# Performance work log

Hardware: AMD Instinct MI355X
Metric: run time of the kernel (lower is better)

The kernel has to match this reference:

```python
import jax, jax.numpy as jnp
import numpy as np

K = 20
EPS = 1e-5


def graph_feature(x, k=K):
    # x: [B, C, N] -> [B, 2C, N, k] (DGCNN edge features)
    xt = jnp.transpose(x, (0, 2, 1))                      # [B, N, C]
    sq = jnp.sum(xt * xt, axis=-1)                        # [B, N]
    inner = jnp.einsum('bnc,bmc->bnm', xt, xt)            # [B, N, N]
    neg_dist = 2.0 * inner - sq[:, :, None] - sq[:, None, :]
    idx = jax.lax.top_k(neg_dist, k)[1]                   # [B, N, k]
    nbr = jax.vmap(lambda f, i: f[i])(xt, idx)            # [B, N, k, C]
    ctr = jnp.broadcast_to(xt[:, :, None, :], nbr.shape)
    feat = jnp.concatenate([nbr - ctr, ctr], axis=-1)     # [B, N, k, 2C]
    return jnp.transpose(feat, (0, 3, 1, 2))              # [B, 2C, N, k]


def conv_bn_relu(x, W, g, b):
    # 1x1 conv (channel matmul) + BatchNorm (batch stats, training mode) + ReLU
    y = jnp.einsum('oc,bcnk->bonk', W, x)
    m = jnp.mean(y, axis=(0, 2, 3), keepdims=True)
    v = jnp.var(y, axis=(0, 2, 3), keepdims=True)
    yn = (y - m) * jax.lax.rsqrt(v + EPS)
    return jax.nn.relu(yn * g[None, :, None, None] + b[None, :, None, None])


def setup_inputs() -> dict:
    key = jax.random.key(0)
    ks = jax.random.split(key, 12)
    d = {'x': jax.random.normal(ks[0], (8, 3, 2048), dtype=jnp.float32)}
    chans = [(6, 64), (64, 64), (64, 128), (128, 256), (512, 512)]
    for i, (cin, cout) in enumerate(chans):
        d[f'W{i+1}'] = jax.random.normal(ks[i + 1], (cout, cin), dtype=jnp.float32) * (1.0 / np.sqrt(cin))
        d[f'g{i+1}'] = jnp.ones((cout,), dtype=jnp.float32)
        d[f'b{i+1}'] = jnp.zeros((cout,), dtype=jnp.float32)
    return d


def reference(x, W1, g1, b1, W2, g2, b2, W3, g3, b3, W4, g4, b4, W5, g5, b5):
    B, C, N = x.shape
    h = graph_feature(x)                                  # [B, 6, N, k]
    h = conv_bn_relu(h, W1, g1, b1)
    x1 = jnp.max(h, axis=-1, keepdims=True)               # [B, 64, N, 1]
    h = conv_bn_relu(h, W2, g2, b2)
    x2 = jnp.max(h, axis=-1, keepdims=True)
    h = conv_bn_relu(h, W3, g3, b3)
    x3 = jnp.max(h, axis=-1, keepdims=True)
    h = conv_bn_relu(h, W4, g4, b4)
    x4 = jnp.max(h, axis=-1, keepdims=True)
    cat = jnp.concatenate([x1, x2, x3, x4], axis=1)       # [B, 512, N, 1]
    out = conv_bn_relu(cat, W5, g5, b5)                   # [B, 512, N, 1]
    return out.reshape(B, -1, N)
```

## Files before the change

### kernel.cpp

```cpp
#include <hip/hip_runtime.h>
#include <hip/hip_bf16.h>

typedef _Float16 f16;
typedef _Float16 f16x8 __attribute__((ext_vector_type(8)));
typedef _Float16 f16x4 __attribute__((ext_vector_type(4)));
typedef float    f32x4 __attribute__((ext_vector_type(4)));
typedef unsigned long long u64;

constexpr int NB  = 8;
constexpr int NPT = 2048;
constexpr int KK  = 20;
constexpr int PT  = NB * NPT * KK;
constexpr int BNP = NB * NPT;
constexpr float EPS_BN = 1e-5f;
constexpr int NREP = 64;

constexpr size_t OFF_IDX = 0;
constexpr size_t OFF_WT1 = OFF_IDX + (size_t)BNP * KK * 4;
constexpr size_t OFF_WH2 = OFF_WT1 + 384 * 4;
constexpr size_t OFF_WH3 = OFF_WH2 + 4096 * 2;
constexpr size_t OFF_WH4 = OFF_WH3 + 8192 * 2;
constexpr size_t OFF_WH5 = OFF_WH4 + 32768 * 2;
constexpr size_t OFF_ST  = OFF_WH5 + 262144 * 2;
constexpr size_t OFF_SS  = OFF_ST + 5 * 1024 * 4;
constexpr size_t OFF_CAT = OFF_SS + 5 * 1024 * 4;
constexpr size_t OFF_Y3  = OFF_CAT + (size_t)BNP * 512 * 2;
constexpr size_t OFF_Y1  = OFF_Y3 + (size_t)PT * 64 * 2;
constexpr size_t OFF_Y2  = OFF_Y3 + (size_t)PT * 128 * 2;
constexpr size_t OFF_REP = OFF_Y2 + (size_t)PT * 64 * 2;
constexpr size_t WS_NEED = OFF_REP + (size_t)NREP * 1024 * 4;

__global__ void marker_kernel(float* __restrict__ out, float v) {
    if (threadIdx.x == 0 && blockIdx.x == 0) out[0] = v;
}

__device__ __forceinline__ void gload16(const f16* g, f16* ldsbase) {
    __builtin_amdgcn_global_load_lds(
        (const __attribute__((address_space(1))) void*)g,
        (__attribute__((address_space(3))) void*)ldsbase, 16, 0, 0);
}

__global__ __launch_bounds__(256) void prep_weights(
        const float* __restrict__ W1, const float* __restrict__ W2,
        const float* __restrict__ W3, const float* __restrict__ W4,
        const float* __restrict__ W5,
        float* __restrict__ wt1, f16* __restrict__ wh2, f16* __restrict__ wh3,
        f16* __restrict__ wh4, f16* __restrict__ wh5) {
    int i = blockIdx.x * 256 + threadIdx.x;
    if (i < 384)    { int o = i / 6, c = i - o * 6; wt1[c * 64 + o] = W1[i]; }
    if (i < 4096)   wh2[i] = (f16)W2[i];
    if (i < 8192)   wh3[i] = (f16)W3[i];
    if (i < 32768)  wh4[i] = (f16)W4[i];
    if (i < 262144) wh5[i] = (f16)W5[i];
}

__device__ __forceinline__ float distf(const float* __restrict__ xb, int m,
                                       float xn0, float xn1, float xn2, float sqn) {
    float xm0 = xb[m], xm1 = xb[NPT + m], xm2 = xb[2 * NPT + m];
    float dot = xn0 * xm0 + xn1 * xm1 + xn2 * xm2;
    float sqm = xm0 * xm0 + xm1 * xm1 + xm2 * xm2;
    return 2.f * dot - sqn - sqm;
}
__device__ __forceinline__ u64 mkkey(float d, int m) {
    unsigned u = __float_as_uint(d);
    u = (u & 0x80000000u) ? ~u : (u | 0x80000000u);
    return ((u64)u << 32) | (unsigned)(2047 - m);
}
__device__ __forceinline__ int key2m(u64 k) { return 2047 - (int)(k & 0xFFFFFFFFull); }

__device__ __forceinline__ void qins(u64 k, u64& q0, u64& q1, u64& q2, u64& q3, u64& spill) {
    bool c0 = k > q0, c1 = k > q1, c2 = k > q2, c3 = k > q3;
    u64 drop = c3 ? q3 : k;
    spill = spill > drop ? spill : drop;
    q3 = c2 ? q2 : (c3 ? k : q3);
    q2 = c1 ? q1 : (c2 ? k : q2);
    q1 = c0 ? q0 : (c1 ? k : q1);
    q0 = c0 ? k  : q0;
}

__global__ __launch_bounds__(256) void knn_kernel(const float* __restrict__ x,
                                                  int* __restrict__ idxo) {
    const int lane = threadIdx.x & 63;
    const int wid  = threadIdx.x >> 6;
    const int r    = blockIdx.x * 4 + wid;
    const int b    = r >> 11;
    const int n    = r & 2047;
    const float* xb = x + b * (3 * NPT);

    const float xn0 = xb[n], xn1 = xb[NPT + n], xn2 = xb[2 * NPT + n];
    const float sqn = xn0 * xn0 + xn1 * xn1 + xn2 * xn2;

    u64 q0 = 0, q1 = 0, q2 = 0, q3 = 0, spill = 0;
#pragma unroll
    for (int i = 0; i < 32; ++i) {
        int m = i * 64 + lane;
        qins(mkkey(distf(xb, m, xn0, xn1, xn2, sqn), m), q0, q1, q2, q3, spill);
    }

    __shared__ int cand[4][32];
    int C;

    unsigned lo = 0u, hi = 0xFFFFFFFFu;
#pragma unroll 1
    for (int it = 0; it < 32 && lo < hi; ++it) {
        unsigned span = hi - lo;
        unsigned mid  = lo + (span >> 1) + (span & 1);
        u64 M = (u64)mid << 32;
        int cnt = __popcll(__ballot(q0 >= M)) + __popcll(__ballot(q1 >= M))
                + __popcll(__ballot(q2 >= M)) + __popcll(__ballot(q3 >= M));
        if (cnt >= 26) lo = mid; else hi = mid - 1;
    }
    const u64 T64 = (u64)lo << 32;

    u64 b0 = __ballot(q0 >= T64), b1 = __ballot(q1 >= T64);
    u64 b2 = __ballot(q2 >= T64), b3 = __ballot(q3 >= T64);
    int n0 = __popcll(b0), n1 = __popcll(b1), n2 = __popcll(b2), n3 = __popcll(b3);
    C = n0 + n1 + n2 + n3;
    bool conflict = (__ballot(spill >= T64) != 0ull) || (C > 32);

    if (!conflict) {
        u64 ltm = (1ull << lane) - 1ull;
        if (q0 >= T64) cand[wid][__popcll(b0 & ltm)] = key2m(q0);
        if (q1 >= T64) cand[wid][n0 + __popcll(b1 & ltm)] = key2m(q1);
        if (q2 >= T64) cand[wid][n0 + n1 + __popcll(b2 & ltm)] = key2m(q2);
        if (q3 >= T64) cand[wid][n0 + n1 + n2 + __popcll(b3 & ltm)] = key2m(q3);
    } else {
        C = 26;
#pragma unroll 1
        for (int t = 0; t < 26; ++t) {
            u64 v = q0;
#pragma unroll
            for (int s = 1; s < 64; s <<= 1) {
                u64 ov = __shfl_xor(v, s);
                if (ov > v) v = ov;
            }
            if (lane == 0) cand[wid][t] = key2m(v);
            if (q0 == v) {
                q0 = q1; q1 = q2; q2 = q3; q3 = 0;
                if (!(q0 > spill)) {
                    q0 = q1 = q2 = q3 = 0; spill = 0;
                    for (int ii = 0; ii < 32; ++ii) {
                        int mr = ii * 64 + lane;
                        u64 kr = mkkey(distf(xb, mr, xn0, xn1, xn2, sqn), mr);
                        if (kr < v) qins(kr, q0, q1, q2, q3, spill);
                    }
                }
            }
        }
    }
    __syncthreads();

    int mm = (lane < C) ? cand[wid][lane] : 0;
    const double dxn0 = (double)xn0, dxn1 = (double)xn1, dxn2 = (double)xn2;
    const double dsqn = dxn0 * dxn0 + dxn1 * dxn1 + dxn2 * dxn2;
    double xm0 = (double)xb[mm], xm1 = (double)xb[NPT + mm], xm2 = (double)xb[2 * NPT + mm];
    double ddot = dxn0 * xm0 + dxn1 * xm1 + dxn2 * xm2;
    double dsqm = xm0 * xm0 + xm1 * xm1 + xm2 * xm2;
    double dd   = 2.0 * ddot - dsqn - dsqm;

    int rank = 0;
#pragma unroll 1
    for (int s = 0; s < C; ++s) {
        double ds = __shfl(dd, s);
        int    ms = __shfl(mm, s);
        if (ds > dd || (ds == dd && ms < mm)) ++rank;
    }
    if (lane < C && rank < KK) idxo[rank * BNP + r] = mm;
}

__global__ __launch_bounds__(256) void conv1_kernel(const float* __restrict__ x,
                                                    const int* __restrict__ idx,
                                                    const float* __restrict__ Wt,
                                                    f16* __restrict__ y,
                                                    float* __restrict__ strep) {
    const int tid = threadIdx.x, lane = tid & 63, wid = tid >> 6;
    int p = blockIdx.x * 256 + tid;
    int r = p & (BNP - 1);
    int n = r & 2047;
    int b = r >> 11;
    int m = idx[p];
    const float* xb = x + b * (3 * NPT);
    float f3 = xb[n], f4 = xb[NPT + n], f5 = xb[2 * NPT + n];
    float f0 = xb[m] - f3, f1 = xb[NPT + m] - f4, f2 = xb[2 * NPT + m] - f5;
    float fv[6] = { f0, f1, f2, f3, f4, f5 };

    float acc[64];
#pragma unroll
    for (int o = 0; o < 64; ++o) acc[o] = 0.f;
#pragma unroll
    for (int c = 0; c < 6; ++c) {
        float hv = fv[c];
#pragma unroll
        for (int o = 0; o < 64; ++o) acc[o] = fmaf(Wt[c * 64 + o], hv, acc[o]);
    }
    f16* yp = y + (size_t)p * 64;
#pragma unroll
    for (int o = 0; o < 64; ++o) yp[o] = (f16)acc[o];

    __shared__ float lsum[4][64], lsq[4][64];
#pragma unroll
    for (int o = 0; o < 64; ++o) {
        float s = acc[o], q = acc[o] * acc[o];
#pragma unroll
        for (int off = 32; off >= 1; off >>= 1) { s += __shfl_xor(s, off); q += __shfl_xor(q, off); }
        if (lane == 0) { lsum[wid][o] = s; lsq[wid][o] = q; }
    }
    __syncthreads();
    float* rep = strep + ((blockIdx.x & (NREP - 1)) << 10);
    if (tid < 64) {
        atomicAdd(rep + tid,       lsum[0][tid] + lsum[1][tid] + lsum[2][tid] + lsum[3][tid]);
        atomicAdd(rep + 512 + tid, lsq[0][tid] + lsq[1][tid] + lsq[2][tid] + lsq[3][tid]);
    }
}

template<int CIN, int OBW>
__global__ __launch_bounds__(256) void conv_mfma_kernel(const f16* __restrict__ h,
                                                        const f16* __restrict__ W,
                                                        const float* __restrict__ scshIn,
                                                        f16* __restrict__ y,
                                                        float* __restrict__ strep) {
    constexpr int COUT = OBW * 64;
    const int tid = threadIdx.x, lane = tid & 63, wid = tid >> 6;
    const int lr = lane & 15, lg = lane >> 4;
    const int p0 = blockIdx.x * (256 / OBW) + (wid / OBW) * 64;
    const int ob = (wid & (OBW - 1)) * 64;

    f16x8 Bn[CIN / 32][4];
#pragma unroll
    for (int kt = 0; kt < CIN / 32; ++kt) {
        const int koff = kt * 32 + lg * 8;
        const float4 s0 = *(const float4*)(scshIn + koff);
        const float4 s1 = *(const float4*)(scshIn + koff + 4);
        const float4 h0 = *(const float4*)(scshIn + 512 + koff);
        const float4 h1 = *(const float4*)(scshIn + 512 + koff + 4);
        const float scr[8] = { s0.x, s0.y, s0.z, s0.w, s1.x, s1.y, s1.z, s1.w };
        const float shr[8] = { h0.x, h0.y, h0.z, h0.w, h1.x, h1.y, h1.z, h1.w };
#pragma unroll
        for (int pt = 0; pt < 4; ++pt) {
            f16x8 raw = *(const f16x8*)(h + (size_t)(p0 + pt * 16 + lr) * CIN + koff);
            f16x8 Bv;
#pragma unroll
            for (int e = 0; e < 8; ++e)
                Bv[e] = (f16)fmaxf(fmaf((float)raw[e], scr[e], shr[e]), 0.f);
            Bn[kt][pt] = Bv;
        }
    }

    f32x4 acc[4][4];
#pragma unroll
    for (int pt = 0; pt < 4; ++pt)
#pragma unroll
        for (int t = 0; t < 4; ++t) acc[pt][t] = (f32x4){0.f, 0.f, 0.f, 0.f};

#pragma unroll
    for (int kt = 0; kt < CIN / 32; ++kt) {
        const int koff = kt * 32 + lg * 8;
        f16x8 A[4];
#pragma unroll
        for (int t = 0; t < 4; ++t)
            A[t] = *(const f16x8*)(W + (size_t)(ob + 16 * t + lr) * CIN + koff);
#pragma unroll
        for (int pt = 0; pt < 4; ++pt)
#pragma unroll
            for (int t = 0; t < 4; ++t)
                acc[pt][t] = __builtin_amdgcn_mfma_f32_16x16x32_f16(A[t], Bn[kt][pt], acc[pt][t], 0, 0, 0);
    }
#pragma unroll
    for (int pt = 0; pt < 4; ++pt) {
        int px = p0 + pt * 16 + lr;
#pragma unroll
        for (int t = 0; t < 4; ++t) {
            f16x4 v;
            v[0] = (f16)acc[pt][t][0]; v[1] = (f16)acc[pt][t][1];
            v[2] = (f16)acc[pt][t][2]; v[3] = (f16)acc[pt][t][3];
            *(f16x4*)(y + (size_t)px * COUT + ob + 16 * t + 4 * lg) = v;
        }
    }
    __shared__ float lsum[4][64], lsq[4][64];
#pragma unroll
    for (int t = 0; t < 4; ++t)
#pragma unroll
        for (int j = 0; j < 4; ++j) {
            float s = acc[0][t][j] + acc[1][t][j] + acc[2][t][j] + acc[3][t][j];
            float q = acc[0][t][j] * acc[0][t][j] + acc[1][t][j] * acc[1][t][j]
                    + acc[2][t][j] * acc[2][t][j] + acc[3][t][j] * acc[3][t][j];
#pragma unroll
            for (int m2 = 1; m2 < 16; m2 <<= 1) { s += __shfl_xor(s, m2); q += __shfl_xor(q, m2); }
            if (lr == 0) { lsum[wid][16 * t + 4 * lg + j] = s; lsq[wid][16 * t + 4 * lg + j] = q; }
        }
    __syncthreads();
    float* rep = strep + ((blockIdx.x & (NREP - 1)) << 10);
    if (tid < COUT) {
        int obIdx = tid >> 6, c = tid & 63;
        float S = 0.f, Q = 0.f;
#pragma unroll
        for (int w = obIdx; w < 4; w += OBW) { S += lsum[w][c]; Q += lsq[w][c]; }
        atomicAdd(rep + tid, S);
        atomicAdd(rep + 512 + tid, Q);
    }
}

__global__ __launch_bounds__(256) void conv4_fused_mfma(const f16* __restrict__ h,
                                                        const f16* __restrict__ W,
                                                        const float* __restrict__ scshIn,
                                                        float* __restrict__ strep,
                                                        f16* __restrict__ mx4,
                                                        f16* __restrict__ mn4,
                                                        f16* __restrict__ cat) {
    const int tid = threadIdx.x, lane = tid & 63, wid = tid >> 6;
    const int lr = lane & 15, lg = lane >> 4;
    const int r0 = blockIdx.x * 16;
    const int ob = wid * 64;

    __shared__ f16 sb[2][4][16][128];

    f32x4 rmax[4], rmin[4], rsum[4], rsq[4];
#pragma unroll
    for (int t = 0; t < 4; ++t) {
        rmax[t] = (f32x4){-3.3e38f, -3.3e38f, -3.3e38f, -3.3e38f};
        rmin[t] = (f32x4){ 3.3e38f,  3.3e38f,  3.3e38f,  3.3e38f};
        rsum[t] = (f32x4){0.f, 0.f, 0.f, 0.f};
        rsq[t]  = (f32x4){0.f, 0.f, 0.f, 0.f};
    }
    f16x8 im[4];
#pragma unroll
    for (int kt = 0; kt < 4; ++kt)
#pragma unroll
        for (int e = 0; e < 8; ++e) im[kt][e] = (f16)0.f;

    auto STAGE = [&](int buf, int kc) {
        const f16* gk = h + ((size_t)(kc * 4 + wid) * BNP + r0) * 128;
#pragma unroll
        for (int i = 0; i < 4; ++i) {
            int rr = i * 4 + (lane >> 4);
            int cc = (lane & 15) ^ rr;
            gload16(gk + (size_t)rr * 128 + cc * 8, &sb[buf][wid][i * 4][0]);
        }
    };

    STAGE(0, 0);
    __syncthreads();

    int cur = 0;
#pragma unroll 1
    for (int kc = 0; kc < 5; ++kc) {
        if (kc < 4) STAGE(cur ^ 1, kc + 1);

        f32x4 acc[4][4];
#pragma unroll
        for (int pt = 0; pt < 4; ++pt)
#pragma unroll
            for (int t = 0; t < 4; ++t) acc[pt][t] = (f32x4){0.f, 0.f, 0.f, 0.f};

#pragma unroll
        for (int kt = 0; kt < 4; ++kt) {
            const int koff = kt * 32 + lg * 8;
            const float4 s0 = *(const float4*)(scshIn + koff);
            const float4 s1 = *(const float4*)(scshIn + koff + 4);
            const float4 h0 = *(const float4*)(scshIn + 512 + koff);
            const float4 h1 = *(const float4*)(scshIn + 512 + koff + 4);
            const float scr[8] = { s0.x, s0.y, s0.z, s0.w, s1.x, s1.y, s1.z, s1.w };
            const float shr[8] = { h0.x, h0.y, h0.z, h0.w, h1.x, h1.y, h1.z, h1.w };
            f16x8 A[4];
#pragma unroll
            for (int t = 0; t < 4; ++t)
                A[t] = *(const f16x8*)(W + (size_t)(ob + 16 * t + lr) * 128 + koff);
            f16x8 Bv[4];
#pragma unroll
            for (int pt = 0; pt < 4; ++pt) {
                int cpos = (kt * 4 + lg) ^ lr;
                f16x8 raw = *(const f16x8*)(&sb[cur][pt][lr][cpos * 8]);
                f16x8 Bn;
#pragma unroll
                for (int e = 0; e < 8; ++e)
                    Bn[e] = (f16)fmaxf(fmaf((float)raw[e], scr[e], shr[e]), 0.f);
                Bv[pt] = Bn;
            }
#pragma unroll
            for (int pt = 0; pt < 4; ++pt)
#pragma unroll
                for (int e = 0; e < 8; ++e)
                    im[kt][e] = (Bv[pt][e] > im[kt][e]) ? Bv[pt][e] : im[kt][e];
#pragma unroll
            for (int pt = 0; pt < 4; ++pt)
#pragma unroll
                for (int t = 0; t < 4; ++t)
                    acc[pt][t] = __builtin_amdgcn_mfma_f32_16x16x32_f16(A[t], Bv[pt], acc[pt][t], 0, 0, 0);
        }
#pragma unroll
        for (int pt = 0; pt < 4; ++pt)
#pragma unroll
            for (int t = 0; t < 4; ++t)
#pragma unroll
                for (int j = 0; j < 4; ++j) {
                    float v = acc[pt][t][j];
                    rmax[t][j] = fmaxf(rmax[t][j], v);
                    rmin[t][j] = fminf(rmin[t][j], v);
                    rsum[t][j] += v;
                    rsq[t][j]  += v * v;
                }
        __syncthreads();
        cur ^= 1;
    }

    if (wid == 0) {
#pragma unroll
        for (int kt = 0; kt < 4; ++kt)
            *(f16x8*)(cat + (size_t)(r0 + lr) * 512 + 128 + kt * 32 + lg * 8) = im[kt];
    }
#pragma unroll
    for (int t = 0; t < 4; ++t) {
        f16x4 vx, vn;
#pragma unroll
        for (int j = 0; j < 4; ++j) { vx[j] = (f16)rmax[t][j]; vn[j] = (f16)rmin[t][j]; }
        size_t base = (size_t)(r0 + lr) * 256 + ob + 16 * t + 4 * lg;
        *(f16x4*)(mx4 + base) = vx;
        *(f16x4*)(mn4 + base) = vn;
    }
    float* rep = strep + ((blockIdx.x & (NREP - 1)) << 10);
#pragma unroll
    for (int t = 0; t < 4; ++t)
#pragma unroll
        for (int j = 0; j < 4; ++j) {
            float s = rsum[t][j], q = rsq[t][j];
#pragma unroll
            for (int m2 = 1; m2 < 16; m2 <<= 1) { s += __shfl_xor(s, m2); q += __shfl_xor(q, m2); }
            if (lr == 0) {
                atomicAdd(rep + ob + 16 * t + 4 * lg + j, s);
                atomicAdd(rep + 512 + ob + 16 * t + 4 * lg + j, q);
            }
        }
}

__global__ __launch_bounds__(256) void cat4_kernel(const f16* __restrict__ mx4,
                                                   const f16* __restrict__ mn4,
                                                   const float* __restrict__ scsh,
                                                   f16* __restrict__ cat) {
    int i = blockIdx.x * 256 + threadIdx.x;
    int r = i >> 8, ch = i & 255;
    float sc = scsh[ch], sh = scsh[512 + ch];
    float v  = (sc > 0.f) ? (float)mx4[i] : (float)mn4[i];
    cat[(size_t)r * 512 + 256 + ch] = (f16)fmaxf(fmaf(v, sc, sh), 0.f);
}

__global__ __launch_bounds__(256) void conv5_mfma(const f16* __restrict__ cat,
                                                  const f16* __restrict__ W,
                                                  float* __restrict__ out,
                                                  float* __restrict__ strep) {
    const int tid = threadIdx.x;
    const int lane = tid & 63, wid = tid >> 6;
    const int lr = lane & 15, lg = lane >> 4;
    const int p0 = blockIdx.x * 64;
    const int ob = blockIdx.y * 256 + wid * 64;

    f32x4 acc[4][4];
#pragma unroll
    for (int pt = 0; pt < 4; ++pt)
#pragma unroll
        for (int t = 0; t < 4; ++t) acc[pt][t] = (f32x4){0.f, 0.f, 0.f, 0.f};

#pragma unroll
    for (int kt = 0; kt < 16; ++kt) {
        const int koff = kt * 32 + lg * 8;
        f16x8 A[4];
#pragma unroll
        for (int t = 0; t < 4; ++t)
            A[t] = *(const f16x8*)(W + (size_t)(ob + 16 * t + lr) * 512 + koff);
#pragma unroll
        for (int pt = 0; pt < 4; ++pt) {
            f16x8 B = *(const f16x8*)(cat + (size_t)(p0 + pt * 16 + lr) * 512 + koff);
#pragma unroll
            for (int t = 0; t < 4; ++t)
                acc[pt][t] = __builtin_amdgcn_mfma_f32_16x16x32_f16(A[t], B, acc[pt][t], 0, 0, 0);
        }
    }
#pragma unroll
    for (int pt = 0; pt < 4; ++pt) {
        int px = p0 + pt * 16 + lr;
        int b = px >> 11, n = px & 2047;
#pragma unroll
        for (int t = 0; t < 4; ++t) {
#pragma unroll
            for (int j = 0; j < 4; ++j) {
                int o = ob + 16 * t + 4 * lg + j;
                out[((size_t)(b * 512 + o)) * 2048 + n] = acc[pt][t][j];
            }
        }
    }
    __shared__ float lsum[4][64], lsq[4][64];
#pragma unroll
    for (int t = 0; t < 4; ++t)
#pragma unroll
        for (int j = 0; j < 4; ++j) {
            float s = acc[0][t][j] + acc[1][t][j] + acc[2][t][j] + acc[3][t][j];
            float q = acc[0][t][j] * acc[0][t][j] + acc[1][t][j] * acc[1][t][j]
                    + acc[2][t][j] * acc[2][t][j] + acc[3][t][j] * acc[3][t][j];
#pragma unroll
            for (int m2 = 1; m2 < 16; m2 <<= 1) { s += __shfl_xor(s, m2); q += __shfl_xor(q, m2); }
            if (lr == 0) { lsum[wid][16 * t + 4 * lg + j] = s; lsq[wid][16 * t + 4 * lg + j] = q; }
        }
    __syncthreads();
    float* rep = strep + ((blockIdx.x & (NREP - 1)) << 10);
    if (tid < 256) {
        int w = tid >> 6, c = tid & 63;
        atomicAdd(rep + blockIdx.y * 256 + tid, lsum[w][c]);
        atomicAdd(rep + 512 + blockIdx.y * 256 + tid, lsq[w][c]);
    }
}

__global__ void finalize_kernel(const float* __restrict__ strep, const float* __restrict__ g,
                                const float* __restrict__ bb, float* __restrict__ scsh,
                                int C, float invM) {
    int c = threadIdx.x;
    if (c < C) {
        float s = 0.f, q = 0.f;
#pragma unroll 4
        for (int rr = 0; rr < NREP; ++rr) {
            s += strep[rr * 1024 + c];
            q += strep[rr * 1024 + 512 + c];
        }
        float mean = s * invM;
        float var  = q * invM - mean * mean;
        float istd = rsqrtf(var + EPS_BN);
        float sc   = g[c] * istd;
        scsh[c]       = sc;
        scsh[512 + c] = bb[c] - mean * sc;
    }
}

template<int C>
__global__ __launch_bounds__(256) void catmax_vec(const f16* __restrict__ y,
                                                  const float* __restrict__ scsh,
                                                  f16* __restrict__ cat, int coff) {
    constexpr int CB = C / 8;
    int i  = blockIdx.x * 256 + threadIdx.x;
    int r  = i / CB;
    int cc = (i - r * CB) * 8;
    float sc[8], sh[8];
#pragma unroll
    for (int e = 0; e < 8; ++e) { sc[e] = scsh[cc + e]; sh[e] = scsh[512 + cc + e]; }
    float mx[8];
#pragma unroll
    for (int e = 0; e < 8; ++e) mx[e] = -3.3e38f;
#pragma unroll
    for (int k = 0; k < KK; ++k) {
        f16x8 v = *(const f16x8*)(y + ((size_t)k * BNP + r) * C + cc);
#pragma unroll
        for (int e = 0; e < 8; ++e)
            mx[e] = fmaxf(mx[e], fmaf((float)v[e], sc[e], sh[e]));
    }
    f16x8 o;
#pragma unroll
    for (int e = 0; e < 8; ++e) o[e] = (f16)fmaxf(mx[e], 0.f);
    *(f16x8*)(cat + (size_t)r * 512 + coff + cc) = o;
}

__global__ __launch_bounds__(256) void norm5_kernel(float* __restrict__ out,
                                                    const float* __restrict__ scsh) {
    int o = blockIdx.y;
    int r = blockIdx.x * 256 + threadIdx.x;
    int b = r >> 11, n = r & 2047;
    float sc = scsh[o], sh = scsh[512 + o];
    size_t i = ((size_t)(b * 512 + o)) * 2048 + n;
    float v = fmaf(out[i], sc, sh);
    out[i] = v > 0.f ? v : 0.f;
}

extern "C" void kernel_launch(void* const* d_in, const int* in_sizes, int n_in,
                              void* d_out, int out_size, void* d_ws, size_t ws_size,
                              hipStream_t stream) {
    float* out = (float*)d_out;
    if (ws_size < WS_NEED) {
        marker_kernel<<<1, 64, 0, stream>>>(out, 1000.0f + (float)(ws_size >> 20));
        return;
    }

    const float* x  = (const float*)d_in[0];
    const float* W1 = (const float*)d_in[1];
    const float* g1 = (const float*)d_in[2];
    const float* b1 = (const float*)d_in[3];
    const float* W2 = (const float*)d_in[4];
    const float* g2 = (const float*)d_in[5];
    const float* b2 = (const float*)d_in[6];
    const float* W3 = (const float*)d_in[7];
    const float* g3 = (const float*)d_in[8];
    const float* b3 = (const float*)d_in[9];
    const float* W4 = (const float*)d_in[10];
    const float* g4 = (const float*)d_in[11];
    const float* b4 = (const float*)d_in[12];
    const float* W5 = (const float*)d_in[13];
    const float* g5 = (const float*)d_in[14];
    const float* b5 = (const float*)d_in[15];

    char*  ws    = (char*)d_ws;
    int*   idx   = (int*)(ws + OFF_IDX);
    float* wt1   = (float*)(ws + OFF_WT1);
    f16*   wh2   = (f16*)(ws + OFF_WH2);
    f16*   wh3   = (f16*)(ws + OFF_WH3);
    f16*   wh4   = (f16*)(ws + OFF_WH4);
    f16*   wh5   = (f16*)(ws + OFF_WH5);
    float* scsh  = (float*)(ws + OFF_SS);
    f16*   cat   = (f16*)(ws + OFF_CAT);
    f16*   y1    = (f16*)(ws + OFF_Y1);
    f16*   y2    = (f16*)(ws + OFF_Y2);
    f16*   y3    = (f16*)(ws + OFF_Y3);
    f16*   mx4   = (f16*)(ws + OFF_Y2);
    f16*   mn4   = (f16*)(ws + OFF_Y2 + (size_t)BNP * 256 * 2);
    float* strep = (float*)(ws + OFF_REP);

    constexpr size_t REP_BYTES = (size_t)NREP * 1024 * 4;
    hipMemsetAsync(strep, 0, REP_BYTES, stream);

    prep_weights<<<1024, 256, 0, stream>>>(W1, W2, W3, W4, W5, wt1, wh2, wh3, wh4, wh5);
    knn_kernel<<<4096, 256, 0, stream>>>(x, idx);

    const float invM  = 1.0f / (float)PT;
    const float invM5 = 1.0f / (float)BNP;

    conv1_kernel<<<PT / 256, 256, 0, stream>>>(x, idx, wt1, y1, strep);
    finalize_kernel<<<1, 512, 0, stream>>>(strep, g1, b1, scsh + 0, 64, invM);
    hipMemsetAsync(strep, 0, REP_BYTES, stream);
    catmax_vec<64><<<BNP * 8 / 256, 256, 0, stream>>>(y1, scsh + 0, cat, 0);

    conv_mfma_kernel<64, 1><<<PT / 256, 256, 0, stream>>>(y1, wh2, scsh + 0, y2, strep);
    finalize_kernel<<<1, 512, 0, stream>>>(strep, g2, b2, scsh + 1024, 64, invM);
    hipMemsetAsync(strep, 0, REP_BYTES, stream);
    catmax_vec<64><<<BNP * 8 / 256, 256, 0, stream>>>(y2, scsh + 1024, cat, 64);

    conv_mfma_kernel<64, 2><<<PT / 128, 256, 0, stream>>>(y2, wh3, scsh + 1024, y3, strep);
    finalize_kernel<<<1, 512, 0, stream>>>(strep, g3, b3, scsh + 2048, 128, invM);
    hipMemsetAsync(strep, 0, REP_BYTES, stream);

    conv4_fused_mfma<<<BNP / 16, 256, 0, stream>>>(y3, wh4, scsh + 2048, strep, mx4, mn4, cat);
    finalize_kernel<<<1, 512, 0, stream>>>(strep, g4, b4, scsh + 3072, 256, invM);
    hipMemsetAsync(strep, 0, REP_BYTES, stream);
    cat4_kernel<<<BNP, 256, 0, stream>>>(mx4, mn4, scsh + 3072, cat);

    conv5_mfma<<<dim3(BNP / 64, 2), 256, 0, stream>>>(cat, wh5, out, strep);
    finalize_kernel<<<1, 512, 0, stream>>>(strep, g5, b5, scsh + 4096, 512, invM5);
    norm5_kernel<<<dim3(BNP / 256, 512), 256, 0, stream>>>(out, scsh + 4096);
}
```

Baseline: 415.0 us.

## Cache squared norms in LDS for kNN, use packed fp16 BN, fold stat reset

The kNN kernel precomputes squared norms of all points into shared memory and scans candidates with two independent top-4 queues that are merged afterwards, to shorten dependency chains. The conv kernels now apply BN scale/shift and ReLU with packed fp16 vector math, using fp16 copies of the scale/shift written by the finalize kernel. Finalize also zeroes the stats replicas itself, which removes the separate memset launches between layers. Doing the normalization in fp16 lowers precision, and every block now does the redundant norm precompute for all 2048 points.

```diff
diff --git a/kernel.cpp b/kernel.cpp
--- a/kernel.cpp
+++ b/kernel.cpp
@@ -54,13 +54,6 @@
     if (i < 262144) wh5[i] = (f16)W5[i];
 }
 
-__device__ __forceinline__ float distf(const float* __restrict__ xb, int m,
-                                       float xn0, float xn1, float xn2, float sqn) {
-    float xm0 = xb[m], xm1 = xb[NPT + m], xm2 = xb[2 * NPT + m];
-    float dot = xn0 * xm0 + xn1 * xm1 + xn2 * xm2;
-    float sqm = xm0 * xm0 + xm1 * xm1 + xm2 * xm2;
-    return 2.f * dot - sqn - sqm;
-}
 __device__ __forceinline__ u64 mkkey(float d, int m) {
     unsigned u = __float_as_uint(d);
     u = (u & 0x80000000u) ? ~u : (u | 0x80000000u);
@@ -80,26 +73,54 @@
 
 __global__ __launch_bounds__(256) void knn_kernel(const float* __restrict__ x,
                                                   int* __restrict__ idxo) {
-    const int lane = threadIdx.x & 63;
-    const int wid  = threadIdx.x >> 6;
+    const int tid  = threadIdx.x;
+    const int lane = tid & 63;
+    const int wid  = tid >> 6;
     const int r    = blockIdx.x * 4 + wid;
     const int b    = r >> 11;
     const int n    = r & 2047;
     const float* xb = x + b * (3 * NPT);
 
+    __shared__ float sqs[NPT];
+    __shared__ int   cand[4][32];
+#pragma unroll
+    for (int i = 0; i < NPT / 256; ++i) {
+        int m = i * 256 + tid;
+        float a0 = xb[m], a1 = xb[NPT + m], a2 = xb[2 * NPT + m];
+        sqs[m] = __fadd_rn(__fadd_rn(__fmul_rn(a0, a0), __fmul_rn(a1, a1)),
+                           __fmul_rn(a2, a2));
+    }
+    __syncthreads();
+
     const float xn0 = xb[n], xn1 = xb[NPT + n], xn2 = xb[2 * NPT + n];
-    const float sqn = xn0 * xn0 + xn1 * xn1 + xn2 * xn2;
-
-    u64 q0 = 0, q1 = 0, q2 = 0, q3 = 0, spill = 0;
-#pragma unroll
-    for (int i = 0; i < 32; ++i) {
-        int m = i * 64 + lane;
-        qins(mkkey(distf(xb, m, xn0, xn1, xn2, sqn), m), q0, q1, q2, q3, spill);
-    }
-
-    __shared__ int cand[4][32];
+    const float sqn = sqs[n];
+
+    auto dist2 = [&](int m) -> float {
+        float dot = __fmaf_rn(xn0, xb[m],
+                    __fmaf_rn(xn1, xb[NPT + m],
+                    __fmul_rn(xn2, xb[2 * NPT + m])));
+        return __fsub_rn(__fsub_rn(__fmul_rn(2.f, dot), sqn), sqs[m]);
+    };
+
+    u64 qa0 = 0, qa1 = 0, qa2 = 0, qa3 = 0, sA = 0;
+    u64 qb0 = 0, qb1 = 0, qb2 = 0, qb3 = 0, sB = 0;
+#pragma unroll
+    for (int i = 0; i < 16; ++i) {
+        int ma = i * 64 + lane;
+        int mb = 1024 + ma;
+        float da = dist2(ma);
+        float db = dist2(mb);
+        qins(mkkey(da, ma), qa0, qa1, qa2, qa3, sA);
+        qins(mkkey(db, mb), qb0, qb1, qb2, qb3, sB);
+    }
+    u64 spill = sA > sB ? sA : sB;
+    qins(qb0, qa0, qa1, qa2, qa3, spill);
+    qins(qb1, qa0, qa1, qa2, qa3, spill);
+    qins(qb2, qa0, qa1, qa2, qa3, spill);
+    qins(qb3, qa0, qa1, qa2, qa3, spill);
+    u64 q0 = qa0, q1 = qa1, q2 = qa2, q3 = qa3;
+
     int C;
-
     unsigned lo = 0u, hi = 0xFFFFFFFFu;
 #pragma unroll 1
     for (int it = 0; it < 32 && lo < hi; ++it) {
@@ -141,7 +162,7 @@
                     q0 = q1 = q2 = q3 = 0; spill = 0;
                     for (int ii = 0; ii < 32; ++ii) {
                         int mr = ii * 64 + lane;
-                        u64 kr = mkkey(distf(xb, mr, xn0, xn1, xn2, sqn), mr);
+                        u64 kr = mkkey(dist2(mr), mr);
                         if (kr < v) qins(kr, q0, q1, q2, q3, spill);
                     }
                 }
@@ -216,7 +237,7 @@
 template<int CIN, int OBW>
 __global__ __launch_bounds__(256) void conv_mfma_kernel(const f16* __restrict__ h,
                                                         const f16* __restrict__ W,
-                                                        const float* __restrict__ scshIn,
+                                                        const f16* __restrict__ scshH,
                                                         f16* __restrict__ y,
                                                         float* __restrict__ strep) {
     constexpr int COUT = OBW * 64;
@@ -229,19 +250,16 @@
 #pragma unroll
     for (int kt = 0; kt < CIN / 32; ++kt) {
         const int koff = kt * 32 + lg * 8;
-        const float4 s0 = *(const float4*)(scshIn + koff);
-        const float4 s1 = *(const float4*)(scshIn + koff + 4);
-        const float4 h0 = *(const float4*)(scshIn + 512 + koff);
-        const float4 h1 = *(const float4*)(scshIn + 512 + koff + 4);
-        const float scr[8] = { s0.x, s0.y, s0.z, s0.w, s1.x, s1.y, s1.z, s1.w };
-        const float shr[8] = { h0.x, h0.y, h0.z, h0.w, h1.x, h1.y, h1.z, h1.w };
+        f16x8 scf = *(const f16x8*)(scshH + koff);
+        f16x8 shf = *(const f16x8*)(scshH + 512 + koff);
 #pragma unroll
         for (int pt = 0; pt < 4; ++pt) {
             f16x8 raw = *(const f16x8*)(h + (size_t)(p0 + pt * 16 + lr) * CIN + koff);
+            f16x8 t = raw * scf + shf;
             f16x8 Bv;
 #pragma unroll
             for (int e = 0; e < 8; ++e)
-                Bv[e] = (f16)fmaxf(fmaf((float)raw[e], scr[e], shr[e]), 0.f);
+                Bv[e] = t[e] > (f16)0.f ? t[e] : (f16)0.f;
             Bn[kt][pt] = Bv;
         }
     }
@@ -302,7 +320,7 @@
 
 __global__ __launch_bounds__(256) void conv4_fused_mfma(const f16* __restrict__ h,
                                                         const f16* __restrict__ W,
-                                                        const float* __restrict__ scshIn,
+                                                        const f16* __restrict__ scshH,
                                                         float* __restrict__ strep,
                                                         f16* __restrict__ mx4,
                                                         f16* __restrict__ mn4,
@@ -355,12 +373,8 @@
 #pragma unroll
         for (int kt = 0; kt < 4; ++kt) {
             const int koff = kt * 32 + lg * 8;
-            const float4 s0 = *(const float4*)(scshIn + koff);
-            const float4 s1 = *(const float4*)(scshIn + koff + 4);
-            const float4 h0 = *(const float4*)(scshIn + 512 + koff);
-            const float4 h1 = *(const float4*)(scshIn + 512 + koff + 4);
-            const float scr[8] = { s0.x, s0.y, s0.z, s0.w, s1.x, s1.y, s1.z, s1.w };
-            const float shr[8] = { h0.x, h0.y, h0.z, h0.w, h1.x, h1.y, h1.z, h1.w };
+            f16x8 scf = *(const f16x8*)(scshH + koff);
+            f16x8 shf = *(const f16x8*)(scshH + 512 + koff);
             f16x8 A[4];
 #pragma unroll
             for (int t = 0; t < 4; ++t)
@@ -370,10 +384,11 @@
             for (int pt = 0; pt < 4; ++pt) {
                 int cpos = (kt * 4 + lg) ^ lr;
                 f16x8 raw = *(const f16x8*)(&sb[cur][pt][lr][cpos * 8]);
+                f16x8 t = raw * scf + shf;
                 f16x8 Bn;
 #pragma unroll
                 for (int e = 0; e < 8; ++e)
-                    Bn[e] = (f16)fmaxf(fmaf((float)raw[e], scr[e], shr[e]), 0.f);
+                    Bn[e] = t[e] > (f16)0.f ? t[e] : (f16)0.f;
                 Bv[pt] = Bn;
             }
 #pragma unroll
@@ -508,9 +523,9 @@
     }
 }
 
-__global__ void finalize_kernel(const float* __restrict__ strep, const float* __restrict__ g,
+__global__ void finalize_kernel(float* __restrict__ strep, const float* __restrict__ g,
                                 const float* __restrict__ bb, float* __restrict__ scsh,
-                                int C, float invM) {
+                                f16* __restrict__ scshH, int C, float invM) {
     int c = threadIdx.x;
     if (c < C) {
         float s = 0.f, q = 0.f;
@@ -519,12 +534,20 @@
             s += strep[rr * 1024 + c];
             q += strep[rr * 1024 + 512 + c];
         }
+#pragma unroll 4
+        for (int rr = 0; rr < NREP; ++rr) {
+            strep[rr * 1024 + c] = 0.f;
+            strep[rr * 1024 + 512 + c] = 0.f;
+        }
         float mean = s * invM;
         float var  = q * invM - mean * mean;
         float istd = rsqrtf(var + EPS_BN);
         float sc   = g[c] * istd;
-        scsh[c]       = sc;
-        scsh[512 + c] = bb[c] - mean * sc;
+        float sh   = bb[c] - mean * sc;
+        scsh[c]        = sc;
+        scsh[512 + c]  = sh;
+        scshH[c]       = (f16)sc;
+        scshH[512 + c] = (f16)sh;
     }
 }
 
@@ -599,6 +622,7 @@
     f16*   wh3   = (f16*)(ws + OFF_WH3);
     f16*   wh4   = (f16*)(ws + OFF_WH4);
     f16*   wh5   = (f16*)(ws + OFF_WH5);
+    f16*   scshH = (f16*)(ws + OFF_ST);
     float* scsh  = (float*)(ws + OFF_SS);
     f16*   cat   = (f16*)(ws + OFF_CAT);
     f16*   y1    = (f16*)(ws + OFF_Y1);
@@ -608,8 +632,7 @@
     f16*   mn4   = (f16*)(ws + OFF_Y2 + (size_t)BNP * 256 * 2);
     float* strep = (float*)(ws + OFF_REP);
 
-    constexpr size_t REP_BYTES = (size_t)NREP * 1024 * 4;
-    hipMemsetAsync(strep, 0, REP_BYTES, stream);
+    hipMemsetAsync(strep, 0, (size_t)NREP * 1024 * 4, stream);
 
     prep_weights<<<1024, 256, 0, stream>>>(W1, W2, W3, W4, W5, wt1, wh2, wh3, wh4, wh5);
     knn_kernel<<<4096, 256, 0, stream>>>(x, idx);
@@ -618,25 +641,21 @@
     const float invM5 = 1.0f / (float)BNP;
 
     conv1_kernel<<<PT / 256, 256, 0, stream>>>(x, idx, wt1, y1, strep);
-    finalize_kernel<<<1, 512, 0, stream>>>(strep, g1, b1, scsh + 0, 64, invM);
-    hipMemsetAsync(strep, 0, REP_BYTES, stream);
+    finalize_kernel<<<1, 512, 0, stream>>>(strep, g1, b1, scsh + 0, scshH + 0, 64, invM);
     catmax_vec<64><<<BNP * 8 / 256, 256, 0, stream>>>(y1, scsh + 0, cat, 0);
 
-    conv_mfma_kernel<64, 1><<<PT / 256, 256, 0, stream>>>(y1, wh2, scsh + 0, y2, strep);
-    finalize_kernel<<<1, 512, 0, stream>>>(strep, g2, b2, scsh + 1024, 64, invM);
-    hipMemsetAsync(strep, 0, REP_BYTES, stream);
+    conv_mfma_kernel<64, 1><<<PT / 256, 256, 0, stream>>>(y1, wh2, scshH + 0, y2, strep);
+    finalize_kernel<<<1, 512, 0, stream>>>(strep, g2, b2, scsh + 1024, scshH + 1024, 64, invM);
     catmax_vec<64><<<BNP * 8 / 256, 256, 0, stream>>>(y2, scsh + 1024, cat, 64);
 
-    conv_mfma_kernel<64, 2><<<PT / 128, 256, 0, stream>>>(y2, wh3, scsh + 1024, y3, strep);
-    finalize_kernel<<<1, 512, 0, stream>>>(strep, g3, b3, scsh + 2048, 128, invM);
-    hipMemsetAsync(strep, 0, REP_BYTES, stream);
-
-    conv4_fused_mfma<<<BNP / 16, 256, 0, stream>>>(y3, wh4, scsh + 2048, strep, mx4, mn4, cat);
-    finalize_kernel<<<1, 512, 0, stream>>>(strep, g4, b4, scsh + 3072, 256, invM);
-    hipMemsetAsync(strep, 0, REP_BYTES, stream);
+    conv_mfma_kernel<64, 2><<<PT / 128, 256, 0, stream>>>(y2, wh3, scshH + 1024, y3, strep);
+    finalize_kernel<<<1, 512, 0, stream>>>(strep, g3, b3, scsh + 2048, scshH + 2048, 128, invM);
+
+    conv4_fused_mfma<<<BNP / 16, 256, 0, stream>>>(y3, wh4, scshH + 2048, strep, mx4, mn4, cat);
+    finalize_kernel<<<1, 512, 0, stream>>>(strep, g4, b4, scsh + 3072, scshH + 3072, 256, invM);
     cat4_kernel<<<BNP, 256, 0, stream>>>(mx4, mn4, scsh + 3072, cat);
 
     conv5_mfma<<<dim3(BNP / 64, 2), 256, 0, stream>>>(cat, wh5, out, strep);
-    finalize_kernel<<<1, 512, 0, stream>>>(strep, g5, b5, scsh + 4096, 512, invM5);
+    finalize_kernel<<<1, 512, 0, stream>>>(strep, g5, b5, scsh + 4096, scshH + 4096, 512, invM5);
     norm5_kernel<<<dim3(BNP / 256, 512), 256, 0, stream>>>(out, scsh + 4096);
 }
```

Result: faster. 401.8 us (-3.2%).
